# Kernel tuning notes

Measured on AMD Instinct MI355X. Metric: run time of the kernel, lower is better.

The kernel has to match this reference:

```python
import jax, jax.numpy as jnp
import numpy as np

# Problem sizes (packed acts shape = [B*T*(S+1), V])
B, T, S, V = 8, 400, 40, 512
BLANK = 0  # blank_label init kwarg
NEG_INF = jnp.float32(-1e30)


def setup_inputs() -> dict:
    key = jax.random.key(0)
    k1, k2 = jax.random.split(key)
    acts = jax.random.normal(k1, (B * T * (S + 1), V), dtype=jnp.float32)
    # labels are real (non-blank) symbols in [1, V)
    labels = jax.random.randint(k2, (B, S), 1, V).astype(jnp.int32)
    input_lengths = jnp.full((B,), T, dtype=jnp.int32)
    label_lengths = jnp.full((B,), S, dtype=jnp.int32)
    return {
        "acts": acts,
        "labels": labels,
        "input_lengths": input_lengths,
        "label_lengths": label_lengths,
    }


def _monotonic_rnnt_costs(acts, labels, input_lengths, label_lengths):
    # Module applies softmax internally -> work in log-prob space.
    lp = jax.nn.log_softmax(acts.reshape(B, T, S + 1, V), axis=-1)
    lp_blank = lp[..., BLANK]  # [B, T, S+1]
    # log P(y_{u+1} | t, u) for u in 0..S-1
    lp_label = jnp.take_along_axis(
        lp[:, :, :S, :], labels[:, None, :, None].astype(jnp.int32), axis=3
    )[..., 0]  # [B, T, S]

    # alpha[b, u] = log prob of emitting first u labels using frames processed so far.
    alpha0 = jnp.full((B, S + 1), NEG_INF, dtype=acts.dtype).at[:, 0].set(0.0)

    def step(alpha, xs):
        lpb_t, lpl_t = xs  # [B, S+1], [B, S]
        stay = alpha + lpb_t                 # emit blank: u unchanged
        move = alpha[:, :-1] + lpl_t         # emit label y_{u+1}: u -> u+1
        new = stay.at[:, 1:].set(jnp.logaddexp(stay[:, 1:], move))
        return new, new

    _, alphas = jax.lax.scan(
        step, alpha0, (jnp.swapaxes(lp_blank, 0, 1), jnp.swapaxes(lp_label, 0, 1))
    )  # alphas: [T, B, S+1], alphas[t] = alpha after t+1 frames

    b_idx = jnp.arange(B)
    costs = -alphas[input_lengths - 1, b_idx, label_lengths]  # [B]
    return costs


def reference(acts, labels, input_lengths, label_lengths):
    return _monotonic_rnnt_costs(acts, labels, input_lengths, label_lengths)
```

## Files before the change

### kernel.cpp

```cpp
#include <hip/hip_runtime.h>

#define TB 8
#define TT 400
#define TS 40
#define TV 512
#define SU (TS + 1)
#define NROWS (TB * TT * SU)
#define KCH 16
#define NCH (TT / KCH)
#define NEG_INF (-1.0e30f)
#define INV_LN2 1.44269504088896341f
#define LN2 0.69314718055994531f

__global__ __launch_bounds__(256) void rowlse_kernel(
    const float* __restrict__ acts, const int* __restrict__ labels,
    float* __restrict__ lp_blank, float* __restrict__ lp_label)
{
    const int wave = threadIdx.x >> 6;
    const int lane = threadIdx.x & 63;
    const int row  = blockIdx.x * 4 + wave;

    const float* rp = acts + (size_t)row * TV;
    float4 a = *(const float4*)(rp + lane * 8);
    float4 b = *(const float4*)(rp + lane * 8 + 4);

    float m = fmaxf(fmaxf(fmaxf(a.x, a.y), fmaxf(a.z, a.w)),
                    fmaxf(fmaxf(b.x, b.y), fmaxf(b.z, b.w)));
#pragma unroll
    for (int off = 1; off < 64; off <<= 1) m = fmaxf(m, __shfl_xor(m, off));

    float s = __expf(a.x - m) + __expf(a.y - m) + __expf(a.z - m) + __expf(a.w - m)
            + __expf(b.x - m) + __expf(b.y - m) + __expf(b.z - m) + __expf(b.w - m);
#pragma unroll
    for (int off = 1; off < 64; off <<= 1) s += __shfl_xor(s, off);

    const float logZ = m + logf(s);

    if (lane == 0) {
        const int u  = row % SU;
        const int bt = row / SU;
        lp_blank[row] = (a.x - logZ) * INV_LN2;
        if (u < TS) {
            const int b_idx = bt / TT;
            const int col   = labels[b_idx * TS + u];
            lp_label[bt * TS + u] = (rp[col] - logZ) * INV_LN2;
        }
    }
}

__device__ __forceinline__ float wave_shr1(float x) {
    return __int_as_float(
        __builtin_amdgcn_update_dpp(0, __float_as_int(x), 0x138, 0xf, 0xf, true));
}

__global__ __launch_bounds__(64) void alpha_kernel(
    const float* __restrict__ lp_blank, const float* __restrict__ lp_label,
    const int* __restrict__ input_lengths, const int* __restrict__ label_lengths,
    float* __restrict__ out)
{
    const int b = blockIdx.x;
    const int u = threadIdx.x;

    const int inlen  = input_lengths[b];
    const int lablen = label_lengths[b];

    const int uu = (u <= TS) ? u : TS;
    const int ul = (u >= 1 && u <= TS) ? (u - 1) : 0;
    const float* pb_ptr = lp_blank + (size_t)b * TT * SU + uu;
    const float* pl_ptr = lp_label + (size_t)b * TT * TS + ul;
    const bool u_dead = (u == 0 || u > TS);

    float alpha = (u == 0) ? 0.0f : NEG_INF;
    float saved = NEG_INF;

    float pbA[KCH], plA[KCH], pbB[KCH], plB[KCH];

#define LOADC(PB, PL, C) { \
    _Pragma("unroll") \
    for (int k = 0; k < KCH; ++k) { \
        (PB)[k] = pb_ptr[((C) * KCH + k) * SU]; \
        float plv = pl_ptr[((C) * KCH + k) * TS]; \
        (PL)[k] = u_dead ? NEG_INF : plv; \
    } }

#define COMPUTE(PB, PL, C) { \
    _Pragma("unroll") \
    for (int k = 0; k < KCH; ++k) { \
        const float prev = wave_shr1(alpha); \
        const float stay = alpha + (PB)[k]; \
        const float move = prev + (PL)[k]; \
        const float mx = fmaxf(stay, move); \
        const float mn = fminf(stay, move); \
        alpha = mx + __builtin_amdgcn_logf(1.0f + __builtin_amdgcn_exp2f(mn - mx)); \
        saved = ((C) * KCH + k == inlen - 1) ? alpha : saved; \
    } }

    LOADC(pbA, plA, 0);
    for (int i = 0; i < 12; ++i) {
        const int c0 = 2 * i;
        LOADC(pbB, plB, c0 + 1);
        COMPUTE(pbA, plA, c0);
        LOADC(pbA, plA, c0 + 2);
        COMPUTE(pbB, plB, c0 + 1);
    }
    COMPUTE(pbA, plA, NCH - 1);

#undef LOADC
#undef COMPUTE

    const float cost_alpha = __shfl(saved, lablen);
    if (u == 0) out[b] = -cost_alpha * LN2;
}

extern "C" void kernel_launch(void* const* d_in, const int* in_sizes, int n_in,
                              void* d_out, int out_size, void* d_ws, size_t ws_size,
                              hipStream_t stream) {
    const float* acts          = (const float*)d_in[0];
    const int*   labels        = (const int*)d_in[1];
    const int*   input_lengths = (const int*)d_in[2];
    const int*   label_lengths = (const int*)d_in[3];
    float* out = (float*)d_out;

    float* lp_blank = (float*)d_ws;
    float* lp_label = lp_blank + NROWS;

    rowlse_kernel<<<NROWS / 4, 256, 0, stream>>>(acts, labels, lp_blank, lp_label);
    alpha_kernel<<<TB, 64, 0, stream>>>(lp_blank, lp_label,
                                        input_lengths, label_lengths, out);
}
```

Baseline: 59.13 us.

## Compose four alpha steps into banded transfer matrices to shorten serial scan

```diff
diff --git a/kernel.cpp b/kernel.cpp
--- a/kernel.cpp
+++ b/kernel.cpp
@@ -6,11 +6,30 @@
 #define TV 512
 #define SU (TS + 1)
 #define NROWS (TB * TT * SU)
-#define KCH 16
-#define NCH (TT / KCH)
+#define NSS (TT / 4)
 #define NEG_INF (-1.0e30f)
 #define INV_LN2 1.44269504088896341f
 #define LN2 0.69314718055994531f
+
+__device__ __forceinline__ float wave_shr1(float x) {
+    return __int_as_float(
+        __builtin_amdgcn_update_dpp(0, __float_as_int(x), 0x138, 0xf, 0xf, true));
+}
+
+__device__ __forceinline__ float lse4(float a, float b, float c, float d) {
+    float m = fmaxf(fmaxf(a, b), fmaxf(c, d));
+    float s = __builtin_amdgcn_exp2f(a - m) + __builtin_amdgcn_exp2f(b - m)
+            + __builtin_amdgcn_exp2f(c - m) + __builtin_amdgcn_exp2f(d - m);
+    return m + __builtin_amdgcn_logf(s);
+}
+__device__ __forceinline__ float lse6(float a, float b, float c,
+                                      float d, float e, float f) {
+    float m = fmaxf(fmaxf(fmaxf(a, b), fmaxf(c, d)), fmaxf(e, f));
+    float s = __builtin_amdgcn_exp2f(a - m) + __builtin_amdgcn_exp2f(b - m)
+            + __builtin_amdgcn_exp2f(c - m) + __builtin_amdgcn_exp2f(d - m)
+            + __builtin_amdgcn_exp2f(e - m) + __builtin_amdgcn_exp2f(f - m);
+    return m + __builtin_amdgcn_logf(s);
+}
 
 __global__ __launch_bounds__(256) void rowlse_kernel(
     const float* __restrict__ acts, const int* __restrict__ labels,
@@ -48,12 +67,58 @@
     }
 }
 
-__device__ __forceinline__ float wave_shr1(float x) {
-    return __int_as_float(
-        __builtin_amdgcn_update_dpp(0, __float_as_int(x), 0x138, 0xf, 0xf, true));
-}
-
-__global__ __launch_bounds__(64) void alpha_kernel(
+__global__ __launch_bounds__(256) void compose_kernel(
+    const float* __restrict__ lp_blank, const float* __restrict__ lp_label,
+    float* __restrict__ W)
+{
+    const int wv   = blockIdx.x * 4 + (threadIdx.x >> 6);
+    const int lane = threadIdx.x & 63;
+    const int b = wv / NSS;
+    const int s = wv - b * NSS;
+    const int t0 = s * 4;
+    const int u  = (lane <= TS) ? lane : TS;
+
+    const float* pb = lp_blank + ((size_t)b * TT + t0) * SU + u;
+    const float* pl = lp_label + ((size_t)b * TT + t0) * TS + ((u >= 1) ? u - 1 : 0);
+    const float b0 = pb[0], b1 = pb[SU], b2 = pb[2 * SU], b3 = pb[3 * SU];
+    const float l0 = pl[0], l1 = pl[TS], l2 = pl[2 * TS], l3 = pl[3 * TS];
+
+    const float bm1_0 = wave_shr1(b0), bm1_1 = wave_shr1(b1), bm1_2 = wave_shr1(b2);
+    const float bm2_0 = wave_shr1(bm1_0), bm2_1 = wave_shr1(bm1_1);
+    const float bm3_0 = wave_shr1(bm2_0);
+    const float lm1_0 = wave_shr1(l0), lm1_1 = wave_shr1(l1), lm1_2 = wave_shr1(l2);
+    const float lm2_0 = wave_shr1(lm1_0), lm2_1 = wave_shr1(lm1_1);
+    const float lm3_0 = wave_shr1(lm2_0);
+
+    const float W0 = b0 + b1 + b2 + b3;
+    const float W1 = lse4(l0 + b1 + b2 + b3,
+                          bm1_0 + l1 + b2 + b3,
+                          bm1_0 + bm1_1 + l2 + b3,
+                          bm1_0 + bm1_1 + bm1_2 + l3);
+    const float W2 = lse6(lm1_0 + l1 + b2 + b3,
+                          lm1_0 + bm1_1 + l2 + b3,
+                          lm1_0 + bm1_1 + bm1_2 + l3,
+                          bm2_0 + lm1_1 + l2 + b3,
+                          bm2_0 + lm1_1 + bm1_2 + l3,
+                          bm2_0 + bm2_1 + lm1_2 + l3);
+    const float W3 = lse4(bm3_0 + lm2_1 + lm1_2 + l3,
+                          lm2_0 + bm2_1 + lm1_2 + l3,
+                          lm2_0 + lm1_1 + bm1_2 + l3,
+                          lm2_0 + lm1_1 + l2 + b3);
+    const float W4 = lm3_0 + lm2_1 + lm1_2 + l3;
+
+    if (lane <= TS) {
+        float* wp = W + (((size_t)b * NSS + s) * 5) * SU + lane;
+        wp[0 * SU] = W0;
+        wp[1 * SU] = (lane >= 1) ? W1 : NEG_INF;
+        wp[2 * SU] = (lane >= 2) ? W2 : NEG_INF;
+        wp[3 * SU] = (lane >= 3) ? W3 : NEG_INF;
+        wp[4 * SU] = (lane >= 4) ? W4 : NEG_INF;
+    }
+}
+
+__global__ __launch_bounds__(64) void scan_kernel(
+    const float* __restrict__ W,
     const float* __restrict__ lp_blank, const float* __restrict__ lp_label,
     const int* __restrict__ input_lengths, const int* __restrict__ label_lengths,
     float* __restrict__ out)
@@ -63,50 +128,80 @@
 
     const int inlen  = input_lengths[b];
     const int lablen = label_lengths[b];
+    const int rr     = inlen & 3;
+    const int s_part = inlen >> 2;
+    const int s_cap  = (rr == 0) ? (inlen >> 2) - 1 : -1;
 
     const int uu = (u <= TS) ? u : TS;
     const int ul = (u >= 1 && u <= TS) ? (u - 1) : 0;
-    const float* pb_ptr = lp_blank + (size_t)b * TT * SU + uu;
-    const float* pl_ptr = lp_label + (size_t)b * TT * TS + ul;
     const bool u_dead = (u == 0 || u > TS);
+    const float* wbase = W + ((size_t)b * NSS * 5) * SU + uu;
 
     float alpha = (u == 0) ? 0.0f : NEG_INF;
     float saved = NEG_INF;
 
-    float pbA[KCH], plA[KCH], pbB[KCH], plB[KCH];
-
-#define LOADC(PB, PL, C) { \
+    float wA[20], wB[20];
+
+#define LOADG(BUF, G) { \
     _Pragma("unroll") \
-    for (int k = 0; k < KCH; ++k) { \
-        (PB)[k] = pb_ptr[((C) * KCH + k) * SU]; \
-        float plv = pl_ptr[((C) * KCH + k) * TS]; \
-        (PL)[k] = u_dead ? NEG_INF : plv; \
+    for (int ss = 0; ss < 4; ++ss) { \
+        _Pragma("unroll") \
+        for (int j = 0; j < 5; ++j) \
+            (BUF)[ss * 5 + j] = wbase[((size_t)(((G) * 4 + ss) * 5 + j)) * SU]; \
     } }
 
-#define COMPUTE(PB, PL, C) { \
+#define COMPG(BUF, G) { \
     _Pragma("unroll") \
-    for (int k = 0; k < KCH; ++k) { \
-        const float prev = wave_shr1(alpha); \
-        const float stay = alpha + (PB)[k]; \
-        const float move = prev + (PL)[k]; \
-        const float mx = fmaxf(stay, move); \
-        const float mn = fminf(stay, move); \
-        alpha = mx + __builtin_amdgcn_logf(1.0f + __builtin_amdgcn_exp2f(mn - mx)); \
-        saved = ((C) * KCH + k == inlen - 1) ? alpha : saved; \
+    for (int ss = 0; ss < 4; ++ss) { \
+        const int s = (G) * 4 + ss; \
+        if (rr && s == s_part) {  \
+            float a2 = alpha; \
+            _Pragma("unroll") \
+            for (int q = 0; q < 3; ++q) { \
+                if (q < rr) { \
+                    const int t = 4 * s_part + q; \
+                    const float pb = lp_blank[((size_t)b * TT + t) * SU + uu]; \
+                    float pl = lp_label[((size_t)b * TT + t) * TS + ul]; \
+                    pl = u_dead ? NEG_INF : pl; \
+                    const float prev = wave_shr1(a2); \
+                    const float stay = a2 + pb; \
+                    const float move = prev + pl; \
+                    const float mx = fmaxf(stay, move); \
+                    const float mn = fminf(stay, move); \
+                    a2 = mx + __builtin_amdgcn_logf(1.0f + __builtin_amdgcn_exp2f(mn - mx)); \
+                } \
+            } \
+            saved = a2; \
+        } \
+        const float s1 = wave_shr1(alpha); \
+        const float s2 = wave_shr1(s1); \
+        const float s3 = wave_shr1(s2); \
+        const float s4 = wave_shr1(s3); \
+        const float T0 = alpha + (BUF)[ss * 5 + 0]; \
+        const float T1 = s1 + (BUF)[ss * 5 + 1]; \
+        const float T2 = s2 + (BUF)[ss * 5 + 2]; \
+        const float T3 = s3 + (BUF)[ss * 5 + 3]; \
+        const float T4 = s4 + (BUF)[ss * 5 + 4]; \
+        const float M = fmaxf(fmaxf(T0, T1), fmaxf(fmaxf(T2, T3), T4)); \
+        const float sm = __builtin_amdgcn_exp2f(T0 - M) + __builtin_amdgcn_exp2f(T1 - M) \
+                       + __builtin_amdgcn_exp2f(T2 - M) + __builtin_amdgcn_exp2f(T3 - M) \
+                       + __builtin_amdgcn_exp2f(T4 - M); \
+        alpha = M + __builtin_amdgcn_logf(sm); \
+        if (s == s_cap) saved = alpha; \
     } }
 
-    LOADC(pbA, plA, 0);
+    LOADG(wA, 0);
     for (int i = 0; i < 12; ++i) {
-        const int c0 = 2 * i;
-        LOADC(pbB, plB, c0 + 1);
-        COMPUTE(pbA, plA, c0);
-        LOADC(pbA, plA, c0 + 2);
-        COMPUTE(pbB, plB, c0 + 1);
+        const int g0 = 2 * i;
+        LOADG(wB, g0 + 1);
+        COMPG(wA, g0);
+        LOADG(wA, g0 + 2);
+        COMPG(wB, g0 + 1);
     }
-    COMPUTE(pbA, plA, NCH - 1);
-
-#undef LOADC
-#undef COMPUTE
+    COMPG(wA, 24);
+
+#undef LOADG
+#undef COMPG
 
     const float cost_alpha = __shfl(saved, lablen);
     if (u == 0) out[b] = -cost_alpha * LN2;
@@ -123,8 +218,10 @@
 
     float* lp_blank = (float*)d_ws;
     float* lp_label = lp_blank + NROWS;
+    float* W        = lp_label + (size_t)TB * TT * TS;
 
     rowlse_kernel<<<NROWS / 4, 256, 0, stream>>>(acts, labels, lp_blank, lp_label);
-    alpha_kernel<<<TB, 64, 0, stream>>>(lp_blank, lp_label,
-                                        input_lengths, label_lengths, out);
-}
+    compose_kernel<<<TB * NSS / 4, 256, 0, stream>>>(lp_blank, lp_label, W);
+    scan_kernel<<<TB, 64, 0, stream>>>(W, lp_blank, lp_label,
+                                       input_lengths, label_lengths, out);
+}
```

Measured after the change: 58.83 us. About the same (-0.5%).

## Split serial alpha recursion into parallel 8-frame segment composition plus short scan

Applied to the files above, without the earlier changes.

```diff
diff --git a/kernel.cpp b/kernel.cpp
--- a/kernel.cpp
+++ b/kernel.cpp
@@ -6,11 +6,24 @@
 #define TV 512
 #define SU (TS + 1)
 #define NROWS (TB * TT * SU)
-#define KCH 16
-#define NCH (TT / KCH)
+#define SS 8
+#define NSS (TT / SS)
+#define NW (SS + 1)
+#define GRP 5
+#define NGRP (NSS / GRP)
 #define NEG_INF (-1.0e30f)
 #define INV_LN2 1.44269504088896341f
 #define LN2 0.69314718055994531f
+
+__device__ __forceinline__ float wave_shr1(float x) {
+    return __int_as_float(
+        __builtin_amdgcn_update_dpp(0, __float_as_int(x), 0x138, 0xf, 0xf, true));
+}
+
+__device__ __forceinline__ float lse2(float a, float c) {
+    const float mx = fmaxf(a, c), mn = fminf(a, c);
+    return mx + __builtin_amdgcn_logf(1.0f + __builtin_amdgcn_exp2f(mn - mx));
+}
 
 __global__ __launch_bounds__(256) void rowlse_kernel(
     const float* __restrict__ acts, const int* __restrict__ labels,
@@ -48,12 +61,55 @@
     }
 }
 
-__device__ __forceinline__ float wave_shr1(float x) {
-    return __int_as_float(
-        __builtin_amdgcn_update_dpp(0, __float_as_int(x), 0x138, 0xf, 0xf, true));
-}
-
-__global__ __launch_bounds__(64) void alpha_kernel(
+__global__ __launch_bounds__(256) void compose_kernel(
+    const float* __restrict__ lp_blank, const float* __restrict__ lp_label,
+    float* __restrict__ W)
+{
+    const int wv   = blockIdx.x * 4 + (threadIdx.x >> 6);
+    const int lane = threadIdx.x & 63;
+    const int b  = wv / NSS;
+    const int s  = wv - b * NSS;
+    const int t0 = s * SS;
+    const int uu = (lane <= TS) ? lane : TS;
+    const bool have_l = (lane >= 1 && lane <= TS);
+
+    const float* pb = lp_blank + ((size_t)b * TT + t0) * SU + uu;
+    const float* pl = lp_label + ((size_t)b * TT + t0) * TS + (have_l ? lane - 1 : 0);
+
+    float bm[SS], lm[SS];
+#pragma unroll
+    for (int m = 0; m < SS; ++m) {
+        bm[m] = pb[m * SU];
+        float lv = pl[m * TS];
+        lm[m] = have_l ? lv : NEG_INF;
+    }
+
+    float E[NW];
+    E[0] = 0.0f;
+#pragma unroll
+    for (int j = 1; j < NW; ++j) E[j] = NEG_INF;
+
+#pragma unroll
+    for (int m = 0; m < SS; ++m) {
+#pragma unroll
+        for (int jj = 0; jj < NW - 1; ++jj) {
+            const int j = (NW - 1) - jj;
+            if (j <= m + 1)
+                E[j] = lse2(E[j] + bm[m], wave_shr1(E[j - 1]) + lm[m]);
+        }
+        E[0] += bm[m];
+    }
+
+    if (lane <= TS) {
+        float* wp = W + (((size_t)b * NSS + s) * NW) * SU + lane;
+#pragma unroll
+        for (int j = 0; j < NW; ++j)
+            wp[j * SU] = (lane >= j) ? E[j] : NEG_INF;
+    }
+}
+
+__global__ __launch_bounds__(64) void scan_kernel(
+    const float* __restrict__ W,
     const float* __restrict__ lp_blank, const float* __restrict__ lp_label,
     const int* __restrict__ input_lengths, const int* __restrict__ label_lengths,
     float* __restrict__ out)
@@ -63,50 +119,85 @@
 
     const int inlen  = input_lengths[b];
     const int lablen = label_lengths[b];
+    const int rr     = inlen & (SS - 1);
+    const int s_part = inlen >> 3;
+    const int s_cap  = (rr == 0) ? s_part - 1 : -1;
 
     const int uu = (u <= TS) ? u : TS;
     const int ul = (u >= 1 && u <= TS) ? (u - 1) : 0;
-    const float* pb_ptr = lp_blank + (size_t)b * TT * SU + uu;
-    const float* pl_ptr = lp_label + (size_t)b * TT * TS + ul;
     const bool u_dead = (u == 0 || u > TS);
+    const float* wbase = W + ((size_t)b * NSS * NW) * SU + uu;
 
     float alpha = (u == 0) ? 0.0f : NEG_INF;
     float saved = NEG_INF;
 
-    float pbA[KCH], plA[KCH], pbB[KCH], plB[KCH];
-
-#define LOADC(PB, PL, C) { \
+    float wA[GRP * NW], wB[GRP * NW];
+
+#define LOADG(BUF, G) { \
     _Pragma("unroll") \
-    for (int k = 0; k < KCH; ++k) { \
-        (PB)[k] = pb_ptr[((C) * KCH + k) * SU]; \
-        float plv = pl_ptr[((C) * KCH + k) * TS]; \
-        (PL)[k] = u_dead ? NEG_INF : plv; \
+    for (int ss = 0; ss < GRP; ++ss) { \
+        _Pragma("unroll") \
+        for (int j = 0; j < NW; ++j) \
+            (BUF)[ss * NW + j] = wbase[((size_t)((((G) * GRP + ss) * NW) + j)) * SU]; \
     } }
 
-#define COMPUTE(PB, PL, C) { \
+#define COMPG(BUF, G) { \
     _Pragma("unroll") \
-    for (int k = 0; k < KCH; ++k) { \
-        const float prev = wave_shr1(alpha); \
-        const float stay = alpha + (PB)[k]; \
-        const float move = prev + (PL)[k]; \
-        const float mx = fmaxf(stay, move); \
-        const float mn = fminf(stay, move); \
-        alpha = mx + __builtin_amdgcn_logf(1.0f + __builtin_amdgcn_exp2f(mn - mx)); \
-        saved = ((C) * KCH + k == inlen - 1) ? alpha : saved; \
+    for (int ss = 0; ss < GRP; ++ss) { \
+        const int s = (G) * GRP + ss; \
+        if (rr && s == s_part) {  \
+            float a2 = alpha; \
+            _Pragma("unroll") \
+            for (int q = 0; q < SS - 1; ++q) { \
+                if (q < rr) { \
+                    const int t = SS * s_part + q; \
+                    const float pbv = lp_blank[((size_t)b * TT + t) * SU + uu]; \
+                    float plv = lp_label[((size_t)b * TT + t) * TS + ul]; \
+                    plv = u_dead ? NEG_INF : plv; \
+                    const float prev = wave_shr1(a2); \
+                    a2 = lse2(a2 + pbv, prev + plv); \
+                } \
+            } \
+            saved = a2; \
+        } \
+        const float s1 = wave_shr1(alpha), s2 = wave_shr1(s1); \
+        const float s3 = wave_shr1(s2),    s4 = wave_shr1(s3); \
+        const float s5 = wave_shr1(s4),    s6 = wave_shr1(s5); \
+        const float s7 = wave_shr1(s6),    s8 = wave_shr1(s7); \
+        const float T0 = alpha + (BUF)[ss * NW + 0]; \
+        const float T1 = s1 + (BUF)[ss * NW + 1]; \
+        const float T2 = s2 + (BUF)[ss * NW + 2]; \
+        const float T3 = s3 + (BUF)[ss * NW + 3]; \
+        const float T4 = s4 + (BUF)[ss * NW + 4]; \
+        const float T5 = s5 + (BUF)[ss * NW + 5]; \
+        const float T6 = s6 + (BUF)[ss * NW + 6]; \
+        const float T7 = s7 + (BUF)[ss * NW + 7]; \
+        const float T8 = s8 + (BUF)[ss * NW + 8]; \
+        const float M = fmaxf(fmaxf(fmaxf(fmaxf(T0, T1), fmaxf(T2, T3)), \
+                                    fmaxf(fmaxf(T4, T5), fmaxf(T6, T7))), T8); \
+        const float sm = ((__builtin_amdgcn_exp2f(T0 - M) + __builtin_amdgcn_exp2f(T1 - M)) \
+                       +  (__builtin_amdgcn_exp2f(T2 - M) + __builtin_amdgcn_exp2f(T3 - M))) \
+                       + ((__builtin_amdgcn_exp2f(T4 - M) + __builtin_amdgcn_exp2f(T5 - M)) \
+                       +  (__builtin_amdgcn_exp2f(T6 - M) + __builtin_amdgcn_exp2f(T7 - M))) \
+                       +   __builtin_amdgcn_exp2f(T8 - M); \
+        alpha = M + __builtin_amdgcn_logf(sm); \
+        if (s == s_cap) saved = alpha; \
     } }
 
-    LOADC(pbA, plA, 0);
-    for (int i = 0; i < 12; ++i) {
-        const int c0 = 2 * i;
-        LOADC(pbB, plB, c0 + 1);
-        COMPUTE(pbA, plA, c0);
-        LOADC(pbA, plA, c0 + 2);
-        COMPUTE(pbB, plB, c0 + 1);
-    }
-    COMPUTE(pbA, plA, NCH - 1);
-
-#undef LOADC
-#undef COMPUTE
+    LOADG(wA, 0);
+    for (int i = 0; i < 4; ++i) {
+        const int g0 = 2 * i;
+        LOADG(wB, g0 + 1);
+        COMPG(wA, g0);
+        LOADG(wA, g0 + 2);
+        COMPG(wB, g0 + 1);
+    }
+    LOADG(wB, 9);
+    COMPG(wA, 8);
+    COMPG(wB, 9);
+
+#undef LOADG
+#undef COMPG
 
     const float cost_alpha = __shfl(saved, lablen);
     if (u == 0) out[b] = -cost_alpha * LN2;
@@ -123,8 +214,10 @@
 
     float* lp_blank = (float*)d_ws;
     float* lp_label = lp_blank + NROWS;
+    float* W        = lp_label + (size_t)TB * TT * TS;
 
     rowlse_kernel<<<NROWS / 4, 256, 0, stream>>>(acts, labels, lp_blank, lp_label);
-    alpha_kernel<<<TB, 64, 0, stream>>>(lp_blank, lp_label,
-                                        input_lengths, label_lengths, out);
-}
+    compose_kernel<<<TB * NSS / 4, 256, 0, stream>>>(lp_blank, lp_label, W);
+    scan_kernel<<<TB, 64, 0, stream>>>(W, lp_blank, lp_label,
+                                       input_lengths, label_lengths, out);
+}
```

New measurement: 56.58 us. 4.3% less time.
